# Optimization experiments

Hardware: AMD Instinct MI355X
Metric: run time of the kernel (lower is better)

Reference implementation:

```python
import jax, jax.numpy as jnp
import numpy as np
from jax import lax

B, T, D, A = 32, 2048, 1024, 1024

def setup_inputs() -> dict:
    key = jax.random.key(0)
    ks = jax.random.split(key, 8)
    s = 1.0 / np.sqrt(D)
    return {
        "query": jax.random.normal(ks[0], (B, 1, D), jnp.float32),
        "value": jax.random.normal(ks[1], (B, T, D), jnp.float32),
        "last_attn": jax.random.uniform(ks[2], (B, T), jnp.float32),
        "conv_w": jax.random.normal(ks[3], (A, 1, 3), jnp.float32) * 0.1,
        "conv_b": jnp.zeros((A,), jnp.float32),
        "Wq": jax.random.normal(ks[4], (A, D), jnp.float32) * s,
        "Wv": jax.random.normal(ks[5], (A, D), jnp.float32) * s,
        "bias": jax.random.uniform(ks[6], (A,), jnp.float32, -0.1, 0.1),
        "fc_w": jax.random.normal(ks[7], (1, A), jnp.float32) * (1.0 / np.sqrt(A)),
        "fc_b": jnp.zeros((1,), jnp.float32),
    }

def reference(query, value, last_attn, conv_w, conv_b, Wq, Wv, bias, fc_w, fc_b):
    # location conv1d: (B,1,T) -> (B,A,T), kernel 3, pad 1
    loc = lax.conv_general_dilated(
        last_attn[:, None, :], conv_w, window_strides=(1,), padding="SAME",
        dimension_numbers=("NCH", "OIH", "NCH"))
    loc = loc + conv_b[None, :, None]
    loc = jnp.transpose(loc, (0, 2, 1))  # (B, T, A)
    # fused add + bias + tanh; query proj (B,1,A) broadcasts over T
    hidden = jnp.tanh(query @ Wq.T + value @ Wv.T + loc + bias)  # (B, T, A)
    energy = (hidden @ fc_w.T + fc_b)[..., 0]  # (B, T)
    attn = jax.nn.softmax(energy, axis=-1)  # (B, T)
    context = jnp.einsum("bt,btd->bd", attn, value)[:, None, :]  # (B, 1, D)
    return context, attn
```

## Files before the change

### kernel.cpp

```cpp
#include <hip/hip_runtime.h>
#include <stdint.h>

#define AS1 __attribute__((address_space(1)))
#define AS3 __attribute__((address_space(3)))

typedef __bf16 bf16x8 __attribute__((ext_vector_type(8)));
typedef float  f32x4  __attribute__((ext_vector_type(4)));

__global__ __launch_bounds__(256) void cast_bf16(const float* __restrict__ in,
                                                 __bf16* __restrict__ out, int n8) {
    int i = blockIdx.x * 256 + threadIdx.x;
    if (i >= n8) return;
    const float4* p = (const float4*)in + (size_t)i * 2;
    float4 x = p[0], y = p[1];
    bf16x8 v;
    v[0] = (__bf16)x.x; v[1] = (__bf16)x.y; v[2] = (__bf16)x.z; v[3] = (__bf16)x.w;
    v[4] = (__bf16)y.x; v[5] = (__bf16)y.y; v[6] = (__bf16)y.z; v[7] = (__bf16)y.w;
    *((bf16x8*)out + i) = v;
}

__global__ __launch_bounds__(256) void prep_qb2(const float* __restrict__ q,
                                                const float* __restrict__ Wq,
                                                const float* __restrict__ bias,
                                                const float* __restrict__ convb,
                                                float* __restrict__ qb2) {
    int wid  = threadIdx.x >> 6;
    int lane = threadIdx.x & 63;
    int a    = blockIdx.x * 4 + wid;
    const float* wr_ = Wq + (size_t)a * 1024;
    float w[16];
#pragma unroll
    for (int j = 0; j < 16; ++j) w[j] = wr_[lane + 64 * j];
    float bb = bias[a] + convb[a];
    for (int b = 0; b < 32; ++b) {
        const float* qr = q + (size_t)b * 1024;
        float s = 0.f;
#pragma unroll
        for (int j = 0; j < 16; ++j) s += w[j] * qr[lane + 64 * j];
        for (int m = 1; m < 64; m <<= 1) s += __shfl_xor(s, m);
        if (lane == 0) qb2[b * 1024 + a] = s + bb;
    }
}

__global__ __launch_bounds__(512, 2) void gemm_fused(
    const __bf16* __restrict__ Abf,
    const __bf16* __restrict__ Bbf,
    const float*  __restrict__ qb2,
    const float*  __restrict__ la,
    const float*  __restrict__ convw,
    const float*  __restrict__ fcw,
    float* __restrict__ ep)
{
    constexpr int K = 1024, NT = 16;
    __shared__ __bf16 As[2][256 * 64];
    __shared__ __bf16 Bs[2][256 * 64];

    const int tid  = threadIdx.x;
    const int lane = tid & 63;
    const int wid  = tid >> 6;
    const int wr   = wid >> 2, wc = wid & 3;

    const int bid = blockIdx.x;
    const int swz = (bid & 7) * 128 + (bid >> 3);
    const int rt  = swz >> 2;
    const int ct  = swz & 3;
    const int rowBase = rt * 256;
    const int colBase = ct * 256;

    f32x4 acc[8][4] = {};

    auto STAGE_A = [&](int buf, int half, int k0) {
#pragma unroll
        for (int is = 0; is < 2; ++is) {
            int idx16 = half * 1024 + is * 512 + tid;
            int r     = idx16 >> 3;
            int ssw   = (idx16 ^ r) & 7;
            const __bf16* g = Abf + (size_t)(rowBase + r) * K + k0 + ssw * 8;
            __builtin_amdgcn_global_load_lds((AS1 void*)g, (AS3 void*)(&As[buf][idx16 * 8]), 16, 0, 0);
        }
    };
    auto STAGE_B = [&](int buf, int half, int k0) {
#pragma unroll
        for (int is = 0; is < 2; ++is) {
            int idx16 = half * 1024 + is * 512 + tid;
            int r     = idx16 >> 3;
            int ssw   = (idx16 ^ r) & 7;
            const __bf16* g = Bbf + (size_t)(colBase + r) * K + k0 + ssw * 8;
            __builtin_amdgcn_global_load_lds((AS1 void*)g, (AS3 void*)(&Bs[buf][idx16 * 8]), 16, 0, 0);
        }
    };

#define DO_PHASE(bufv, kk, mh, READB, STAGE_STMT)                              \
    {                                                                          \
        if (READB) {                                                           \
            _Pragma("unroll")                                                  \
            for (int ni = 0; ni < 4; ++ni) {                                   \
                int row  = wc * 64 + ni * 16 + (lane & 15);                    \
                int slot = ((kk) * 4 + (lane >> 4)) ^ (row & 7);               \
                bfr[ni][kk] = *(const bf16x8*)(&Bs[bufv][row * 64 + slot * 8]);\
            }                                                                  \
        }                                                                      \
        bf16x8 af[4];                                                          \
        _Pragma("unroll")                                                      \
        for (int i = 0; i < 4; ++i) {                                          \
            int row  = wr * 128 + ((mh) * 4 + i) * 16 + (lane & 15);           \
            int slot = ((kk) * 4 + (lane >> 4)) ^ (row & 7);                   \
            af[i] = *(const bf16x8*)(&As[bufv][row * 64 + slot * 8]);          \
        }                                                                      \
        STAGE_STMT;                                                            \
        __builtin_amdgcn_s_barrier();                                          \
        asm volatile("s_waitcnt lgkmcnt(0)" ::: "memory");                     \
        __builtin_amdgcn_sched_barrier(0);                                     \
        __builtin_amdgcn_s_setprio(1);                                         \
        _Pragma("unroll")                                                      \
        for (int i = 0; i < 4; ++i)                                            \
            _Pragma("unroll")                                                  \
            for (int ni = 0; ni < 4; ++ni)                                     \
                acc[(mh) * 4 + i][ni] = __builtin_amdgcn_mfma_f32_16x16x32_bf16(\
                    af[i], bfr[ni][kk], acc[(mh) * 4 + i][ni], 0, 0, 0);       \
        __builtin_amdgcn_s_setprio(0);                                         \
        __builtin_amdgcn_s_barrier();                                          \
    }

    STAGE_A(0, 0, 0); STAGE_A(0, 1, 0);
    STAGE_B(0, 0, 0); STAGE_B(0, 1, 0);

#pragma unroll 1
    for (int t = 0; t < NT - 1; ++t) {
        const int buf = t & 1;
        const int kn  = (t + 1) * 64;
        __builtin_amdgcn_sched_barrier(0);
        STAGE_A(buf ^ 1, 0, kn);
        __builtin_amdgcn_sched_barrier(0);
        asm volatile("s_waitcnt vmcnt(2)" ::: "memory");
        __builtin_amdgcn_s_barrier();
        __builtin_amdgcn_sched_barrier(0);
        bf16x8 bfr[4][2];
        DO_PHASE(buf, 0, 0, true,  STAGE_A(buf ^ 1, 1, kn));
        DO_PHASE(buf, 0, 1, false, STAGE_B(buf ^ 1, 0, kn));
        DO_PHASE(buf, 1, 0, true,  STAGE_B(buf ^ 1, 1, kn));
        DO_PHASE(buf, 1, 1, false, (void)0);
    }
    {
        asm volatile("s_waitcnt vmcnt(0)" ::: "memory");
        __builtin_amdgcn_s_barrier();
        __builtin_amdgcn_sched_barrier(0);
        bf16x8 bfr[4][2];
        DO_PHASE(1, 0, 0, true,  (void)0);
        DO_PHASE(1, 0, 1, false, (void)0);
        DO_PHASE(1, 1, 0, true,  (void)0);
        DO_PHASE(1, 1, 1, false, (void)0);
    }
#undef DO_PHASE

    const int b     = rowBase >> 11;
    const int tTile = rowBase & 2047;
    const float* lab  = la  + (size_t)b * 2048;
    const float* qrow = qb2 + (size_t)b * 1024;

    float cw0[4], cw1[4], cw2[4], fv[4], qv[4];
#pragma unroll
    for (int ni = 0; ni < 4; ++ni) {
        int a = colBase + wc * 64 + ni * 16 + (lane & 15);
        cw0[ni] = convw[a * 3 + 0];
        cw1[ni] = convw[a * 3 + 1];
        cw2[ni] = convw[a * 3 + 2];
        fv[ni]  = fcw[a];
        qv[ni]  = qrow[a];
    }
    float* eps = (float*)&As[0][0];
    const int g4 = (lane >> 4) * 4;
#pragma unroll
    for (int mi = 0; mi < 8; ++mi) {
#pragma unroll
        for (int j = 0; j < 4; ++j) {
            int rloc = wr * 128 + mi * 16 + g4 + j;
            int t = tTile + rloc;
            float p1 = lab[t];
            float p0 = (t > 0)    ? lab[t - 1] : 0.f;
            float p2 = (t < 2047) ? lab[t + 1] : 0.f;
            float sum = 0.f;
#pragma unroll
            for (int ni = 0; ni < 4; ++ni) {
                float e = acc[mi][ni][j] + qv[ni] + cw0[ni] * p0 + cw1[ni] * p1 + cw2[ni] * p2;
                float h = 1.f - 2.f / (1.f + __expf(2.f * e));
                sum += fv[ni] * h;
            }
            sum += __shfl_xor(sum, 1);
            sum += __shfl_xor(sum, 2);
            sum += __shfl_xor(sum, 4);
            sum += __shfl_xor(sum, 8);
            if ((lane & 15) == 0) eps[rloc * 4 + wc] = sum;
        }
    }
    __syncthreads();
    if (tid < 256) {
        float e = eps[tid * 4 + 0] + eps[tid * 4 + 1] + eps[tid * 4 + 2] + eps[tid * 4 + 3];
        ep[(size_t)ct * 65536 + rowBase + tid] = e;
    }
}

__global__ __launch_bounds__(256) void softmax_rows(const float* __restrict__ ep,
                                                    float* __restrict__ attn) {
    int b = blockIdx.x, tid = threadIdx.x;
    float* o = attn + (size_t)b * 2048;
    __shared__ float red[4], red2[4];

    float e8[8];
#pragma unroll
    for (int k = 0; k < 8; ++k) {
        int t = tid + 256 * k;
        float s = 0.f;
#pragma unroll
        for (int ct = 0; ct < 4; ++ct) s += ep[(size_t)ct * 65536 + b * 2048 + t];
        e8[k] = s;
    }

    float m = -1e30f;
#pragma unroll
    for (int k = 0; k < 8; ++k) m = fmaxf(m, e8[k]);
    for (int s = 1; s < 64; s <<= 1) m = fmaxf(m, __shfl_xor(m, s));
    if ((tid & 63) == 0) red[tid >> 6] = m;
    __syncthreads();
    m = fmaxf(fmaxf(red[0], red[1]), fmaxf(red[2], red[3]));

    float s = 0.f, vals[8];
#pragma unroll
    for (int k = 0; k < 8; ++k) { vals[k] = __expf(e8[k] - m); s += vals[k]; }
    for (int t = 1; t < 64; t <<= 1) s += __shfl_xor(s, t);
    if ((tid & 63) == 0) red2[tid >> 6] = s;
    __syncthreads();
    s = red2[0] + red2[1] + red2[2] + red2[3];
    float inv = 1.f / s;
#pragma unroll
    for (int k = 0; k < 8; ++k) o[tid + 256 * k] = vals[k] * inv;
}

__global__ __launch_bounds__(256) void context_kernel(const float* __restrict__ attn,
                                                      const __bf16* __restrict__ vbf,
                                                      float* __restrict__ ctx) {
    int b = blockIdx.x, tc = blockIdx.y, tid = threadIdx.x;
    int half = tid >> 7, dc = tid & 127;
    const float*  ab = attn + (size_t)b * 2048 + tc * 256 + half * 128;
    const __bf16* vb = vbf + ((size_t)(b * 2048 + tc * 256 + half * 128)) * 1024 + dc * 8;
    float c[8] = {};
#pragma unroll 4
    for (int t = 0; t < 128; ++t) {
        float  w = ab[t];
        bf16x8 v = *(const bf16x8*)(vb + (size_t)t * 1024);
#pragma unroll
        for (int k = 0; k < 8; ++k) c[k] += w * (float)v[k];
    }
    float* out = ctx + (size_t)b * 1024 + dc * 8;
#pragma unroll
    for (int k = 0; k < 8; ++k) atomicAdd(out + k, c[k]);
}

extern "C" void kernel_launch(void* const* d_in, const int* in_sizes, int n_in,
                              void* d_out, int out_size, void* d_ws, size_t ws_size,
                              hipStream_t stream) {
    const float* query     = (const float*)d_in[0];
    const float* value     = (const float*)d_in[1];
    const float* last_attn = (const float*)d_in[2];
    const float* conv_w    = (const float*)d_in[3];
    const float* conv_b    = (const float*)d_in[4];
    const float* Wq        = (const float*)d_in[5];
    const float* Wv        = (const float*)d_in[6];
    const float* bias      = (const float*)d_in[7];
    const float* fc_w      = (const float*)d_in[8];

    float* ctx  = (float*)d_out;
    float* attn = (float*)d_out + 32 * 1024;

    const size_t VBF_B  = (size_t)65536 * 1024 * 2;
    const size_t WVBF_B = (size_t)1024 * 1024 * 2;
    const size_t QB2_B  = (size_t)32 * 1024 * 4;
    const size_t EP_B   = (size_t)4 * 32 * 2048 * 4;
    if (ws_size < VBF_B + WVBF_B + QB2_B + EP_B) return;

    char*   ws   = (char*)d_ws;
    __bf16* vbf  = (__bf16*)ws;
    __bf16* wvbf = (__bf16*)(ws + VBF_B);
    float*  qb2  = (float*)(ws + VBF_B + WVBF_B);
    float*  ep   = (float*)(ws + VBF_B + WVBF_B + QB2_B);

    hipMemsetAsync(ctx, 0, 32 * 1024 * sizeof(float), stream);

    cast_bf16<<<512, 256, 0, stream>>>(Wv, wvbf, 1024 * 1024 / 8);
    prep_qb2<<<256, 256, 0, stream>>>(query, Wq, bias, conv_b, qb2);
    cast_bf16<<<32768, 256, 0, stream>>>(value, vbf, 65536 * 1024 / 8);

    gemm_fused<<<1024, 512, 0, stream>>>(vbf, wvbf, qb2, last_attn, conv_w, fc_w, ep);

    softmax_rows<<<32, 256, 0, stream>>>(ep, attn);
    dim3 gc(32, 8);
    context_kernel<<<gc, 256, 0, stream>>>(attn, vbf, ctx);
}
```

Before: 335.6 us.

## Fuse fp32-to-bf16 cast of value into GEMM A-tile staging

Removes the separate cast kernel for the large value tensor. The GEMM now loads fp32 value tiles into registers, converts them to bf16, and writes them to LDS. The ct==0 column blocks also write the bf16 copy to global memory for the later context kernel. This saves a full extra read and write of the value tensor, but it doubles the fp32 global traffic for A inside the GEMM (four column tiles each reread fp32) and replaces async global_load_lds with a register round trip, which raises register pressure and changes the pipelining schedule.

```diff
diff --git a/kernel.cpp b/kernel.cpp
--- a/kernel.cpp
+++ b/kernel.cpp
@@ -43,13 +43,14 @@
 }
 
 __global__ __launch_bounds__(512, 2) void gemm_fused(
-    const __bf16* __restrict__ Abf,
+    const float*  __restrict__ Af,
     const __bf16* __restrict__ Bbf,
     const float*  __restrict__ qb2,
     const float*  __restrict__ la,
     const float*  __restrict__ convw,
     const float*  __restrict__ fcw,
-    float* __restrict__ ep)
+    float*  __restrict__ ep,
+    __bf16* __restrict__ vbf)
 {
     constexpr int K = 1024, NT = 16;
     __shared__ __bf16 As[2][256 * 64];
@@ -69,48 +70,53 @@
 
     f32x4 acc[8][4] = {};
 
-    auto STAGE_A = [&](int buf, int half, int k0) {
-#pragma unroll
-        for (int is = 0; is < 2; ++is) {
-            int idx16 = half * 1024 + is * 512 + tid;
+    const int sA   = tid & 7;
+    const int rA0  = tid >> 3;
+    const bool emit = (ct == 0);
+
+    auto LOAD_A = [&](int j, int k0, f32x4& x0, f32x4& x1) {
+        int r = j * 64 + rA0;
+        const f32x4* p = (const f32x4*)(Af + (size_t)(rowBase + r) * K + k0) + sA * 2;
+        x0 = p[0]; x1 = p[1];
+    };
+    auto WRITE_A = [&](int buf, int j, int k0, f32x4 x0, f32x4 x1) {
+        int r = j * 64 + rA0;
+        bf16x8 v;
+#pragma unroll
+        for (int e = 0; e < 4; ++e) { v[e] = (__bf16)x0[e]; v[4 + e] = (__bf16)x1[e]; }
+        *(bf16x8*)(&As[buf][r * 64 + (sA ^ (r & 7)) * 8]) = v;
+        if (emit) *(bf16x8*)(vbf + (size_t)(rowBase + r) * K + k0 + sA * 8) = v;
+    };
+    auto STAGE_B = [&](int buf, int k0) {
+#pragma unroll
+        for (int is = 0; is < 4; ++is) {
+            int idx16 = is * 512 + tid;
             int r     = idx16 >> 3;
-            int ssw   = (idx16 ^ r) & 7;
-            const __bf16* g = Abf + (size_t)(rowBase + r) * K + k0 + ssw * 8;
-            __builtin_amdgcn_global_load_lds((AS1 void*)g, (AS3 void*)(&As[buf][idx16 * 8]), 16, 0, 0);
-        }
-    };
-    auto STAGE_B = [&](int buf, int half, int k0) {
-#pragma unroll
-        for (int is = 0; is < 2; ++is) {
-            int idx16 = half * 1024 + is * 512 + tid;
-            int r     = idx16 >> 3;
-            int ssw   = (idx16 ^ r) & 7;
+            int ssw   = (tid ^ r) & 7;
             const __bf16* g = Bbf + (size_t)(colBase + r) * K + k0 + ssw * 8;
             __builtin_amdgcn_global_load_lds((AS1 void*)g, (AS3 void*)(&Bs[buf][idx16 * 8]), 16, 0, 0);
         }
     };
 
-#define DO_PHASE(bufv, kk, mh, READB, STAGE_STMT)                              \
+#define READ_B(bufv, kk)                                                       \
+    _Pragma("unroll")                                                          \
+    for (int ni = 0; ni < 4; ++ni) {                                           \
+        int row  = wc * 64 + ni * 16 + (lane & 15);                            \
+        int slot = (((kk) * 4 + (lane >> 4)) ^ (row & 7));                     \
+        bfr[ni][kk] = *(const bf16x8*)(&Bs[bufv][row * 64 + slot * 8]);        \
+    }
+
+#define PHASE(bufv, kk, mh, PRE, POST)                                         \
     {                                                                          \
-        if (READB) {                                                           \
-            _Pragma("unroll")                                                  \
-            for (int ni = 0; ni < 4; ++ni) {                                   \
-                int row  = wc * 64 + ni * 16 + (lane & 15);                    \
-                int slot = ((kk) * 4 + (lane >> 4)) ^ (row & 7);               \
-                bfr[ni][kk] = *(const bf16x8*)(&Bs[bufv][row * 64 + slot * 8]);\
-            }                                                                  \
-        }                                                                      \
         bf16x8 af[4];                                                          \
         _Pragma("unroll")                                                      \
         for (int i = 0; i < 4; ++i) {                                          \
             int row  = wr * 128 + ((mh) * 4 + i) * 16 + (lane & 15);           \
-            int slot = ((kk) * 4 + (lane >> 4)) ^ (row & 7);                   \
+            int slot = (((kk) * 4 + (lane >> 4)) ^ (row & 7));                 \
             af[i] = *(const bf16x8*)(&As[bufv][row * 64 + slot * 8]);          \
         }                                                                      \
-        STAGE_STMT;                                                            \
+        PRE;                                                                   \
         __builtin_amdgcn_s_barrier();                                          \
-        asm volatile("s_waitcnt lgkmcnt(0)" ::: "memory");                     \
-        __builtin_amdgcn_sched_barrier(0);                                     \
         __builtin_amdgcn_s_setprio(1);                                         \
         _Pragma("unroll")                                                      \
         for (int i = 0; i < 4; ++i)                                            \
@@ -119,39 +125,52 @@
                 acc[(mh) * 4 + i][ni] = __builtin_amdgcn_mfma_f32_16x16x32_bf16(\
                     af[i], bfr[ni][kk], acc[(mh) * 4 + i][ni], 0, 0, 0);       \
         __builtin_amdgcn_s_setprio(0);                                         \
+        POST;                                                                  \
         __builtin_amdgcn_s_barrier();                                          \
     }
 
-    STAGE_A(0, 0, 0); STAGE_A(0, 1, 0);
-    STAGE_B(0, 0, 0); STAGE_B(0, 1, 0);
+    {
+        f32x4 x0[4], x1[4];
+#pragma unroll
+        for (int j = 0; j < 4; ++j) LOAD_A(j, 0, x0[j], x1[j]);
+        STAGE_B(0, 0);
+#pragma unroll
+        for (int j = 0; j < 4; ++j) WRITE_A(0, j, 0, x0[j], x1[j]);
+    }
+    __syncthreads();
 
 #pragma unroll 1
     for (int t = 0; t < NT - 1; ++t) {
         const int buf = t & 1;
         const int kn  = (t + 1) * 64;
-        __builtin_amdgcn_sched_barrier(0);
-        STAGE_A(buf ^ 1, 0, kn);
-        __builtin_amdgcn_sched_barrier(0);
-        asm volatile("s_waitcnt vmcnt(2)" ::: "memory");
-        __builtin_amdgcn_s_barrier();
-        __builtin_amdgcn_sched_barrier(0);
+        asm volatile("" ::: "memory");
+        f32x4 a00, a01, a10, a11, a20, a21, a30, a31;
+        LOAD_A(0, kn, a00, a01);
+        LOAD_A(1, kn, a10, a11);
+        STAGE_B(buf ^ 1, kn);
         bf16x8 bfr[4][2];
-        DO_PHASE(buf, 0, 0, true,  STAGE_A(buf ^ 1, 1, kn));
-        DO_PHASE(buf, 0, 1, false, STAGE_B(buf ^ 1, 0, kn));
-        DO_PHASE(buf, 1, 0, true,  STAGE_B(buf ^ 1, 1, kn));
-        DO_PHASE(buf, 1, 1, false, (void)0);
+        READ_B(buf, 0);
+        PHASE(buf, 0, 0, {}, {});
+        PHASE(buf, 0, 1, { LOAD_A(2, kn, a20, a21); LOAD_A(3, kn, a30, a31); }, {});
+        READ_B(buf, 1);
+        PHASE(buf, 1, 0, { WRITE_A(buf ^ 1, 0, kn, a00, a01);
+                           WRITE_A(buf ^ 1, 1, kn, a10, a11); }, {});
+        PHASE(buf, 1, 1, { WRITE_A(buf ^ 1, 2, kn, a20, a21);
+                           WRITE_A(buf ^ 1, 3, kn, a30, a31); },
+                         { asm volatile("s_waitcnt lgkmcnt(0)" ::: "memory"); });
     }
     {
-        asm volatile("s_waitcnt vmcnt(0)" ::: "memory");
-        __builtin_amdgcn_s_barrier();
-        __builtin_amdgcn_sched_barrier(0);
+        asm volatile("" ::: "memory");
         bf16x8 bfr[4][2];
-        DO_PHASE(1, 0, 0, true,  (void)0);
-        DO_PHASE(1, 0, 1, false, (void)0);
-        DO_PHASE(1, 1, 0, true,  (void)0);
-        DO_PHASE(1, 1, 1, false, (void)0);
-    }
-#undef DO_PHASE
+        READ_B(1, 0);
+        PHASE(1, 0, 0, {}, {});
+        PHASE(1, 0, 1, {}, {});
+        READ_B(1, 1);
+        PHASE(1, 1, 0, {}, {});
+        PHASE(1, 1, 1, {}, {});
+    }
+#undef PHASE
+#undef READ_B
 
     const int b     = rowBase >> 11;
     const int tTile = rowBase & 2047;
@@ -272,25 +291,25 @@
     float* ctx  = (float*)d_out;
     float* attn = (float*)d_out + 32 * 1024;
 
-    const size_t VBF_B  = (size_t)65536 * 1024 * 2;
     const size_t WVBF_B = (size_t)1024 * 1024 * 2;
     const size_t QB2_B  = (size_t)32 * 1024 * 4;
     const size_t EP_B   = (size_t)4 * 32 * 2048 * 4;
-    if (ws_size < VBF_B + WVBF_B + QB2_B + EP_B) return;
+    const size_t VBF_B  = (size_t)65536 * 1024 * 2;
+    if (ws_size < WVBF_B + QB2_B + EP_B + VBF_B) return;
 
     char*   ws   = (char*)d_ws;
-    __bf16* vbf  = (__bf16*)ws;
-    __bf16* wvbf = (__bf16*)(ws + VBF_B);
-    float*  qb2  = (float*)(ws + VBF_B + WVBF_B);
-    float*  ep   = (float*)(ws + VBF_B + WVBF_B + QB2_B);
+    __bf16* wvbf = (__bf16*)ws;
+    float*  qb2  = (float*)(ws + WVBF_B);
+    float*  ep   = (float*)(ws + WVBF_B + QB2_B);
+    __bf16* vbf  = (__bf16*)(ws + WVBF_B + QB2_B + EP_B);
 
     hipMemsetAsync(ctx, 0, 32 * 1024 * sizeof(float), stream);
 
     cast_bf16<<<512, 256, 0, stream>>>(Wv, wvbf, 1024 * 1024 / 8);
     prep_qb2<<<256, 256, 0, stream>>>(query, Wq, bias, conv_b, qb2);
-    cast_bf16<<<32768, 256, 0, stream>>>(value, vbf, 65536 * 1024 / 8);
-
-    gemm_fused<<<1024, 512, 0, stream>>>(vbf, wvbf, qb2, last_attn, conv_w, fc_w, ep);
+
+    gemm_fused<<<1024, 512, 0, stream>>>(value, wvbf, qb2, last_attn, conv_w, fc_w,
+                                         ep, vbf);
 
     softmax_rows<<<32, 256, 0, stream>>>(ep, attn);
     dim3 gc(32, 8);
```

After: 344.9 us. 1.03x slower.
